# Optimization experiments

Measured on AMD Instinct MI355X. Metric: run time of the kernel, lower is better.

Reference implementation:

```python
import jax, jax.numpy as jnp
import numpy as np

EPS = 1e-5
K = 32  # hardcoded k in SamplingGrouping.forward
S1, S2 = 512, 256  # samples


def conv_bn_relu(x, w, gamma, beta):
    # x: [B, C, L]; w: [O, C] (conv1d kernel_size=1, no bias)
    y = jnp.einsum('bcl,oc->bol', x, w)
    # BatchNorm1d in training mode: stats over (batch, length)
    mean = y.mean(axis=(0, 2), keepdims=True)
    var = y.var(axis=(0, 2), keepdims=True)
    yn = (y - mean) * jax.lax.rsqrt(var + EPS)
    return jax.nn.relu(yn * gamma[None, :, None] + beta[None, :, None])


def fps(coords, s):
    # Farthest point sampling; coords [B, N, 3] -> idx [B, s] (deterministic start at 0)
    B, N, _ = coords.shape
    init_idx = jnp.zeros((B,), jnp.int32)

    def body(carry, _):
        dist, last = carry
        p = jnp.take_along_axis(coords, last[:, None, None], axis=1)  # [B,1,3]
        d = jnp.sum((coords - p) ** 2, axis=-1)                        # [B,N]
        dist = jnp.minimum(dist, d)
        nxt = jnp.argmax(dist, axis=-1).astype(jnp.int32)
        return (dist, nxt), nxt

    (_, _), rest = jax.lax.scan(
        body, (jnp.full((B, N), 1e10, coords.dtype), init_idx), None, length=s - 1)
    return jnp.concatenate([init_idx[None, :], rest], axis=0).T  # [B, s]


def index_points(pts, idx):
    # pts [B,N,D], idx [B,...] int -> [B,...,D]
    return jax.vmap(lambda p, i: p[i])(pts, idx)


def sample_and_knn_group(s, k, coords, features):
    # coords [B,N,3], features [B,N,D] -> new_xyz [B,s,3], agg [B,s,k,2D]
    fps_idx = fps(coords, s)
    new_xyz = index_points(coords, fps_idx)      # [B,s,3]
    new_feat = index_points(features, fps_idx)   # [B,s,D]
    # squared distances [B,s,N]
    d = (jnp.sum(new_xyz ** 2, -1, keepdims=True)
         - 2.0 * jnp.einsum('bsc,bnc->bsn', new_xyz, coords)
         + jnp.sum(coords ** 2, -1)[:, None, :])
    _, knn_idx = jax.lax.top_k(-d, k)            # [B,s,k] nearest neighbours
    grouped = index_points(features, knn_idx)    # [B,s,k,D]
    grouped = grouped - new_feat[:, :, None, :]
    agg = jnp.concatenate(
        [grouped, jnp.broadcast_to(new_feat[:, :, None, :], grouped.shape)], axis=-1)
    return new_xyz, agg


def sg_block(s, coords, feats_bcn, wa, ga, ba, wb, gb, bb):
    # SamplingGrouping.forward
    feats = jnp.transpose(feats_bcn, (0, 2, 1))                 # [B,N,D]
    new_xyz, nf = sample_and_knn_group(s, K, coords, feats)     # [B,s,k,2D]
    b, s_, k, d = nf.shape
    nf = jnp.transpose(nf, (0, 1, 3, 2)).reshape(b * s_, d, k)  # [b*s, d, k]
    nf = conv_bn_relu(nf, wa, ga, ba)
    nf = conv_bn_relu(nf, wb, gb, bb)
    nf = nf.max(axis=2)                                         # adaptive_max_pool1d(.,1)
    nf = jnp.transpose(nf.reshape(b, s_, -1), (0, 2, 1))        # [b, O, s]
    return new_xyz, nf


def setup_inputs() -> dict:
    key = jax.random.key(0)
    ks = jax.random.split(key, 8)
    B, N = 32, 8192
    sc = 0.05
    inp = {
        'x': jax.random.normal(ks[0], (B, 3, N), jnp.float32),
        'w1': jax.random.normal(ks[1], (64, 3), jnp.float32) * sc,
        'g1': jnp.ones((64,), jnp.float32), 'b1': jnp.zeros((64,), jnp.float32),
        'w2': jax.random.normal(ks[2], (64, 64), jnp.float32) * sc,
        'g2': jnp.ones((64,), jnp.float32), 'b2': jnp.zeros((64,), jnp.float32),
        's1wa': jax.random.normal(ks[3], (128, 128), jnp.float32) * sc,
        's1ga': jnp.ones((128,), jnp.float32), 's1ba': jnp.zeros((128,), jnp.float32),
        's1wb': jax.random.normal(ks[4], (128, 128), jnp.float32) * sc,
        's1gb': jnp.ones((128,), jnp.float32), 's1bb': jnp.zeros((128,), jnp.float32),
        's2wa': jax.random.normal(ks[5], (256, 256), jnp.float32) * sc,
        's2ga': jnp.ones((256,), jnp.float32), 's2ba': jnp.zeros((256,), jnp.float32),
        's2wb': jax.random.normal(ks[6], (256, 256), jnp.float32) * sc,
        's2gb': jnp.ones((256,), jnp.float32), 's2bb': jnp.zeros((256,), jnp.float32),
    }
    return inp


def reference(x, w1, g1, b1, w2, g2, b2,
              s1wa, s1ga, s1ba, s1wb, s1gb, s1bb,
              s2wa, s2ga, s2ba, s2wb, s2gb, s2bb):
    xyz = jnp.transpose(x[:, :3, :], (0, 2, 1))  # [B,N,3]
    f = conv_bn_relu(x, w1, g1, b1)
    f = conv_bn_relu(f, w2, g2, b2)              # [B,64,N]
    xyz1, f1 = sg_block(S1, xyz, f, s1wa, s1ga, s1ba, s1wb, s1gb, s1bb)   # [B,128,S1]
    _, f2 = sg_block(S2, xyz1, f1, s2wa, s2ga, s2ba, s2wb, s2gb, s2bb)    # [B,256,S2]
    return f2
```

## Files before the change

### kernel.cpp

```cpp
#include <hip/hip_runtime.h>
#include <hip/hip_bf16.h>

#define NB 32
#define NP 8192

__device__ __forceinline__ float dist3(float ax, float ay, float az,
                                       float bx, float by, float bz) {
#pragma clang fp contract(off)
  float dx = ax - bx, dy = ay - by, dz = az - bz;
  return dx * dx + dy * dy + dz * dz;
}
__device__ __forceinline__ float sumsq3(float x, float y, float z) {
#pragma clang fp contract(off)
  return x * x + y * y + z * z;
}
__device__ __forceinline__ float knndist(float qx, float qy, float qz, float qq,
                                         float cx, float cy, float cz) {
#pragma clang fp contract(off)
  float dot = qx * cx + qy * cy + qz * cz;
  float cc = cx * cx + cy * cy + cz * cz;
  return (qq - 2.0f * dot) + cc;
}

__global__ void k_transpose(const float* __restrict__ w, float* __restrict__ wT,
                            int O, int Dd) {
  int i = blockIdx.x * 256 + threadIdx.x;
  if (i < O * Dd) {
    int o = i / Dd, d = i - o * Dd;
    wT[d * O + o] = w[i];
  }
}

__global__ void k_wdiff(const float* __restrict__ w, float* __restrict__ WdT,
                        int O, int D) {
  int i = blockIdx.x * 256 + threadIdx.x;
  if (i < D * O) {
    int d = i / O, o = i - d * O;
    WdT[i] = w[o * 2 * D + D + d] - w[o * 2 * D + d];
  }
}

__global__ __launch_bounds__(256) void k_s1a(const float* __restrict__ x,
                                             const float* __restrict__ w1,
                                             float* __restrict__ xyz,
                                             float* __restrict__ y1) {
  __shared__ float w1s[192];
  int t = threadIdx.x;
  if (t < 192) w1s[t] = w1[t];
  int gid = blockIdx.x * 256 + t;
  int b = gid >> 13, n = gid & (NP - 1);
  __syncthreads();
  const size_t xb = (size_t)b * 3 * NP;
  float x0 = x[xb + n], x1 = x[xb + NP + n], x2 = x[xb + 2 * NP + n];
  xyz[(size_t)gid * 3 + 0] = x0;
  xyz[(size_t)gid * 3 + 1] = x1;
  xyz[(size_t)gid * 3 + 2] = x2;
  float* yo = y1 + (size_t)gid * 64;
#pragma unroll
  for (int o = 0; o < 64; o += 4) {
    float4 v;
    v.x = x0 * w1s[(o + 0) * 3] + x1 * w1s[(o + 0) * 3 + 1] + x2 * w1s[(o + 0) * 3 + 2];
    v.y = x0 * w1s[(o + 1) * 3] + x1 * w1s[(o + 1) * 3 + 1] + x2 * w1s[(o + 1) * 3 + 2];
    v.z = x0 * w1s[(o + 2) * 3] + x1 * w1s[(o + 2) * 3 + 1] + x2 * w1s[(o + 2) * 3 + 2];
    v.w = x0 * w1s[(o + 3) * 3] + x1 * w1s[(o + 3) * 3 + 1] + x2 * w1s[(o + 3) * 3 + 2];
    *(float4*)&yo[o] = v;
  }
}

__global__ __launch_bounds__(256) void k_colstats(const float* __restrict__ buf,
                                                  size_t ME4, float* __restrict__ part) {
  __shared__ float red[128];
  int t = threadIdx.x;
  if (t < 128) red[t] = 0.f;
  float s[4] = {0.f, 0.f, 0.f, 0.f}, q[4] = {0.f, 0.f, 0.f, 0.f};
  size_t stride = (size_t)gridDim.x * 256;
  size_t i0 = (size_t)blockIdx.x * 256 + t;
  int c0 = (int)((i0 * 4) & 63);
  for (size_t i = i0; i < ME4; i += stride) {
    float4 v = ((const float4*)buf)[i];
    s[0] += v.x; q[0] += v.x * v.x;
    s[1] += v.y; q[1] += v.y * v.y;
    s[2] += v.z; q[2] += v.z * v.z;
    s[3] += v.w; q[3] += v.w * v.w;
  }
  __syncthreads();
#pragma unroll
  for (int j = 0; j < 4; ++j) {
    atomicAdd(&red[c0 + j], s[j]);
    atomicAdd(&red[64 + c0 + j], q[j]);
  }
  __syncthreads();
  if (t < 128) atomicAdd(&part[(size_t)(blockIdx.x & 63) * 128 + t], red[t]);
}

__global__ void k_bnfinal(const float* __restrict__ part, const float* __restrict__ gamma,
                          const float* __restrict__ beta, float invcnt, int C,
                          float* __restrict__ sc) {
  int c = threadIdx.x;
  if (c >= C) return;
  float s = 0.f, q = 0.f;
  for (int p = 0; p < 64; ++p) {
    s += part[(size_t)p * 2 * C + c];
    q += part[(size_t)p * 2 * C + C + c];
  }
  float mean = s * invcnt;
  float var = fmaxf(q * invcnt - mean * mean, 0.f);
  float scale = gamma[c] * rsqrtf(var + 1e-5f);
  sc[c] = scale;
  sc[C + c] = beta[c] - mean * scale;
}

__global__ __launch_bounds__(256) void k_s1c(const float* __restrict__ y1,
                                             const float* __restrict__ w2T,
                                             const float* __restrict__ sc1,
                                             float* __restrict__ y2) {
  __shared__ __align__(16) float f1[64 * 65];
  __shared__ __align__(16) float w2s[64 * 64];
  __shared__ float scs[128];
  int t = threadIdx.x;
  if (t < 128) scs[t] = sc1[t];
  for (int i = t; i < 4096; i += 256) w2s[i] = w2T[i];
  size_t base = (size_t)blockIdx.x * 4096;
  __syncthreads();
  for (int i = t; i < 4096; i += 256) {
    int p = i >> 6, c = i & 63;
    float v = y1[base + i];
    v = fmaxf(0.f, v * scs[c] + scs[64 + c]);
    f1[p * 65 + c] = v;
  }
  __syncthreads();
  int pq = t & 15, oq = t >> 4;
  int p0 = pq * 4, o0 = oq * 4;
  float ac[4][4] = {};
  for (int c = 0; c < 64; ++c) {
    float4 wv = *(const float4*)&w2s[c * 64 + o0];
    float a0 = f1[(p0 + 0) * 65 + c];
    float a1 = f1[(p0 + 1) * 65 + c];
    float a2 = f1[(p0 + 2) * 65 + c];
    float a3 = f1[(p0 + 3) * 65 + c];
    ac[0][0] += a0 * wv.x; ac[0][1] += a0 * wv.y; ac[0][2] += a0 * wv.z; ac[0][3] += a0 * wv.w;
    ac[1][0] += a1 * wv.x; ac[1][1] += a1 * wv.y; ac[1][2] += a1 * wv.z; ac[1][3] += a1 * wv.w;
    ac[2][0] += a2 * wv.x; ac[2][1] += a2 * wv.y; ac[2][2] += a2 * wv.z; ac[2][3] += a2 * wv.w;
    ac[3][0] += a3 * wv.x; ac[3][1] += a3 * wv.y; ac[3][2] += a3 * wv.z; ac[3][3] += a3 * wv.w;
  }
#pragma unroll
  for (int i2 = 0; i2 < 4; ++i2) {
    float4 v = {ac[i2][0], ac[i2][1], ac[i2][2], ac[i2][3]};
    *(float4*)&y2[base + (size_t)(p0 + i2) * 64 + o0] = v;
  }
}

__global__ __launch_bounds__(256) void k_s1e(float* __restrict__ y2,
                                             const float* __restrict__ sc2, size_t ME4) {
  __shared__ float scs[128];
  int t = threadIdx.x;
  if (t < 128) scs[t] = sc2[t];
  __syncthreads();
  size_t stride = (size_t)gridDim.x * 256;
  for (size_t i = (size_t)blockIdx.x * 256 + t; i < ME4; i += stride) {
    float4 v = ((float4*)y2)[i];
    int c0 = (int)((i * 4) & 63);
    v.x = fmaxf(0.f, v.x * scs[c0 + 0] + scs[64 + c0 + 0]);
    v.y = fmaxf(0.f, v.y * scs[c0 + 1] + scs[64 + c0 + 1]);
    v.z = fmaxf(0.f, v.z * scs[c0 + 2] + scs[64 + c0 + 2]);
    v.w = fmaxf(0.f, v.w * scs[c0 + 3] + scs[64 + c0 + 3]);
    ((float4*)y2)[i] = v;
  }
}

template <int N, int S, int PPT>
__global__ __launch_bounds__(N / PPT) void k_fps(const float* __restrict__ xyz,
                                                 int* __restrict__ fidx,
                                                 float* __restrict__ sxyz) {
  constexpr int T = N / PPT;
  constexpr int NW = T / 64;
  __shared__ float cl[N * 3];
  __shared__ float wv[2][NW];
  __shared__ int wi[2][NW];
  const int t = threadIdx.x;
  const int b = blockIdx.x;
  const float* base = xyz + (size_t)b * N * 3;
  for (int i = t; i < 3 * N; i += T) cl[i] = base[i];
  __syncthreads();
  float cx[PPT], cy[PPT], cz[PPT], dist[PPT];
#pragma unroll
  for (int j = 0; j < PPT; ++j) {
    int n = t + j * T;
    cx[j] = cl[n * 3 + 0];
    cy[j] = cl[n * 3 + 1];
    cz[j] = cl[n * 3 + 2];
    dist[j] = 1e10f;
  }
  float px = cl[0], py = cl[1], pz = cl[2];
  if (t == 0) {
    fidx[(size_t)b * S] = 0;
    sxyz[(size_t)b * S * 3 + 0] = px;
    sxyz[(size_t)b * S * 3 + 1] = py;
    sxyz[(size_t)b * S * 3 + 2] = pz;
  }
  int par = 0;
  for (int it = 1; it < S; ++it) {
    float bv = -1.0f;
    int bi = 0x7FFFFFFF;
#pragma unroll
    for (int j = 0; j < PPT; ++j) {
      float d = dist3(cx[j], cy[j], cz[j], px, py, pz);
      float dj = fminf(dist[j], d);
      dist[j] = dj;
      if (dj > bv) { bv = dj; bi = t + j * T; }
    }
#pragma unroll
    for (int off = 32; off > 0; off >>= 1) {
      float ov = __shfl_xor(bv, off);
      int oi = __shfl_xor(bi, off);
      if (ov > bv || (ov == bv && oi < bi)) { bv = ov; bi = oi; }
    }
    if ((t & 63) == 0) { wv[par][t >> 6] = bv; wi[par][t >> 6] = bi; }
    __syncthreads();
    float v = wv[par][0];
    int ii = wi[par][0];
#pragma unroll
    for (int w = 1; w < NW; ++w) {
      float ov = wv[par][w];
      int oi = wi[par][w];
      if (ov > v || (ov == v && oi < ii)) { v = ov; ii = oi; }
    }
    px = cl[ii * 3 + 0]; py = cl[ii * 3 + 1]; pz = cl[ii * 3 + 2];
    if (t == 0) {
      fidx[(size_t)b * S + it] = ii;
      sxyz[((size_t)b * S + it) * 3 + 0] = px;
      sxyz[((size_t)b * S + it) * 3 + 1] = py;
      sxyz[((size_t)b * S + it) * 3 + 2] = pz;
    }
    par ^= 1;
  }
}

template <int NPT>
__global__ __launch_bounds__(256) void k_knn(const float* __restrict__ cxyz,
                                             const float* __restrict__ qxyz, int S,
                                             int* __restrict__ knn) {
  constexpr int N = NPT * 256;
  __shared__ float wv[2][4];
  __shared__ int wi[2][4];
  const int t = threadIdx.x;
  const int bs = blockIdx.x;
  const int b = bs / S;
  float qx = qxyz[(size_t)bs * 3 + 0];
  float qy = qxyz[(size_t)bs * 3 + 1];
  float qz = qxyz[(size_t)bs * 3 + 2];
  float qq = sumsq3(qx, qy, qz);
  const float* cb = cxyz + (size_t)b * N * 3;
  float ds[NPT];
  float lmin = 3.0e38f;
  int li = 0x7FFFFFFF;
#pragma unroll
  for (int j = 0; j < NPT; ++j) {
    int n = t + j * 256;
    float d = knndist(qx, qy, qz, qq, cb[(size_t)n * 3], cb[(size_t)n * 3 + 1],
                      cb[(size_t)n * 3 + 2]);
    ds[j] = d;
    if (d < lmin) { lmin = d; li = n; }
  }
  int par = 0;
  for (int r = 0; r < 32; ++r) {
    float bv = lmin;
    int bi = li;
#pragma unroll
    for (int off = 32; off > 0; off >>= 1) {
      float ov = __shfl_xor(bv, off);
      int oi = __shfl_xor(bi, off);
      if (ov < bv || (ov == bv && oi < bi)) { bv = ov; bi = oi; }
    }
    if ((t & 63) == 0) { wv[par][t >> 6] = bv; wi[par][t >> 6] = bi; }
    __syncthreads();
    float v = wv[par][0];
    int ii = wi[par][0];
#pragma unroll
    for (int w = 1; w < 4; ++w) {
      float ov = wv[par][w];
      int oi = wi[par][w];
      if (ov < v || (ov == v && oi < ii)) { v = ov; ii = oi; }
    }
    if (t == 0) knn[(size_t)bs * 32 + r] = ii;
    if (li == ii) {
#pragma unroll
      for (int j = 0; j < NPT; ++j)
        if (t + j * 256 == ii) ds[j] = 3.0e38f;
      lmin = 3.0e38f;
      li = 0x7FFFFFFF;
#pragma unroll
      for (int j = 0; j < NPT; ++j)
        if (ds[j] < lmin) { lmin = ds[j]; li = t + j * 256; }
    }
    par ^= 1;
  }
}

#define KP 36
__device__ __forceinline__ int swzcol(int d, int k) {
  return (k & 3) | ((((unsigned(k) >> 2) ^ (unsigned(d) >> 2)) & 7) << 2);
}

template <int DR, int O, int NT, int CH>
__device__ __forceinline__ void sg_gemm(const float* __restrict__ X,
                                        const float* __restrict__ WT,
                                        float* __restrict__ wch, int t, int o0, int kq,
                                        float (&ac)[4][4]) {
  for (int dc = 0; dc < DR; dc += CH) {
    __syncthreads();
    for (int i = t; i < CH * O; i += NT) wch[i] = WT[(size_t)dc * O + i];
    __syncthreads();
#pragma unroll 8
    for (int dd = 0; dd < CH; ++dd) {
      int d = dc + dd;
      const float4 wvv = *(const float4*)&wch[dd * O + o0];
      const float4 av = *(const float4*)&X[d * KP + ((kq ^ ((d >> 2) & 7)) << 2)];
      ac[0][0] += wvv.x * av.x; ac[0][1] += wvv.x * av.y; ac[0][2] += wvv.x * av.z; ac[0][3] += wvv.x * av.w;
      ac[1][0] += wvv.y * av.x; ac[1][1] += wvv.y * av.y; ac[1][2] += wvv.y * av.z; ac[1][3] += wvv.y * av.w;
      ac[2][0] += wvv.z * av.x; ac[2][1] += wvv.z * av.y; ac[2][2] += wvv.z * av.z; ac[2][3] += wvv.z * av.w;
      ac[3][0] += wvv.w * av.x; ac[3][1] += wvv.w * av.y; ac[3][2] += wvv.w * av.z; ac[3][3] += wvv.w * av.w;
    }
  }
}

template <int D, int NT>
__device__ __forceinline__ void sg_gatherV(const float* __restrict__ f, int Nf, int b,
                                           const int* __restrict__ nidx,
                                           float* __restrict__ V, int t) {
  constexpr int K = 32, DQ = D / 4;
  const float4* f4 = (const float4*)f;
  for (int idx = t; idx < K * DQ; idx += NT) {
    int k = idx / DQ, dq = idx - k * DQ;
    float4 v = f4[((size_t)b * Nf + nidx[k]) * DQ + dq];
    int d0 = dq * 4;
    V[(d0 + 0) * KP + swzcol(d0 + 0, k)] = v.x;
    V[(d0 + 1) * KP + swzcol(d0 + 1, k)] = v.y;
    V[(d0 + 2) * KP + swzcol(d0 + 2, k)] = v.z;
    V[(d0 + 3) * KP + swzcol(d0 + 3, k)] = v.w;
  }
}

template <int D, int O>
__device__ __forceinline__ void sg_corr(const float* __restrict__ WdT,
                                        const float* __restrict__ fqs, int o0, int kq,
                                        float (&c)[4]) {
  c[0] = c[1] = c[2] = c[3] = 0.f;
  for (int d = kq * (D / 8); d < (kq + 1) * (D / 8); ++d) {
    float qv = fqs[d];
    float4 wd = *(const float4*)&WdT[(size_t)d * O + o0];
    c[0] += wd.x * qv; c[1] += wd.y * qv; c[2] += wd.z * qv; c[3] += wd.w * qv;
  }
#pragma unroll
  for (int m = 1; m < 8; m <<= 1) {
    c[0] += __shfl_xor(c[0], m);
    c[1] += __shfl_xor(c[1], m);
    c[2] += __shfl_xor(c[2], m);
    c[3] += __shfl_xor(c[3], m);
  }
}

template <int D, int NT>
__global__ __launch_bounds__(NT) void k_sgA(const float* __restrict__ f, int Nf, int S,
                                            const int* __restrict__ fpsidx,
                                            const int* __restrict__ knn,
                                            const float* __restrict__ waT,
                                            const float* __restrict__ WdT,
                                            float* __restrict__ statsOut) {
  constexpr int D2 = 2 * D, O = D2, K = 32, CH = 16, DQ = D / 4;
  __shared__ __align__(16) float V[D * KP];
  __shared__ __align__(16) float wch[CH * O];
  __shared__ __align__(16) float fqs[D];
  __shared__ int nidx[K];
  __shared__ float red[2 * O];
  const int t = threadIdx.x;
  const int bs = blockIdx.x;
  const int b = bs / S;
  const int qi = fpsidx[bs];
  if (t < K) nidx[t] = knn[(size_t)bs * K + t];
  const float4* f4 = (const float4*)f;
  for (int i = t; i < DQ; i += NT)
    ((float4*)fqs)[i] = f4[((size_t)b * Nf + qi) * DQ + i];
  __syncthreads();
  sg_gatherV<D, NT>(f, Nf, b, nidx, V, t);
  const int oq = t >> 3, kq = t & 7;
  const int o0 = oq * 4;
  float c[4];
  sg_corr<D, O>(WdT, fqs, o0, kq, c);
  float acc[4][4];
#pragma unroll
  for (int i2 = 0; i2 < 4; ++i2)
#pragma unroll
    for (int j = 0; j < 4; ++j) acc[i2][j] = c[i2];
  sg_gemm<D, O, NT, CH>(V, waT, wch, t, o0, kq, acc);
#pragma unroll
  for (int i2 = 0; i2 < 4; ++i2) {
    float sv = acc[i2][0] + acc[i2][1] + acc[i2][2] + acc[i2][3];
    float sq = acc[i2][0] * acc[i2][0] + acc[i2][1] * acc[i2][1] +
               acc[i2][2] * acc[i2][2] + acc[i2][3] * acc[i2][3];
#pragma unroll
    for (int m = 1; m < 8; m <<= 1) {
      sv += __shfl_xor(sv, m);
      sq += __shfl_xor(sq, m);
    }
    if (kq == 0) {
      red[o0 + i2] = sv;
      red[O + o0 + i2] = sq;
    }
  }
  __syncthreads();
  float* slot = statsOut + (size_t)(bs & 63) * (2 * O);
  for (int i = t; i < 2 * O; i += NT) atomicAdd(&slot[i], red[i]);
}

template <int D, int NT>
__global__ __launch_bounds__(NT) void k_sgAB(const float* __restrict__ f, int Nf, int S,
                                             const int* __restrict__ fpsidx,
                                             const int* __restrict__ knn,
                                             const float* __restrict__ waT,
                                             const float* __restrict__ WdT,
                                             const float* __restrict__ wbT,
                                             const float* __restrict__ bnA,
                                             float* __restrict__ statsOut,
                                             float* __restrict__ mm) {
  constexpr int D2 = 2 * D, O = D2, K = 32, CH = 16, DQ = D / 4;
  __shared__ __align__(16) float V[D * KP];
  __shared__ __align__(16) float zb[O * KP];
  __shared__ __align__(16) float wch[CH * O];
  __shared__ __align__(16) float fqs[D];
  __shared__ int nidx[K];
  __shared__ float red[2 * O];
  __shared__ float scb[2 * O];
  const int t = threadIdx.x;
  const int bs = blockIdx.x;
  const int b = bs / S;
  const int qi = fpsidx[bs];
  if (t < K) nidx[t] = knn[(size_t)bs * K + t];
  const float4* f4 = (const float4*)f;
  for (int i = t; i < DQ; i += NT)
    ((float4*)fqs)[i] = f4[((size_t)b * Nf + qi) * DQ + i];
  for (int i = t; i < 2 * O; i += NT) scb[i] = bnA[i];
  __syncthreads();
  sg_gatherV<D, NT>(f, Nf, b, nidx, V, t);
  const int oq = t >> 3, kq = t & 7;
  const int o0 = oq * 4;
  float c[4];
  sg_corr<D, O>(WdT, fqs, o0, kq, c);
  float acc[4][4];
#pragma unroll
  for (int i2 = 0; i2 < 4; ++i2)
#pragma unroll
    for (int j = 0; j < 4; ++j) acc[i2][j] = c[i2];
  sg_gemm<D, O, NT, CH>(V, waT, wch, t, o0, kq, acc);
#pragma unroll
  for (int i2 = 0; i2 < 4; ++i2) {
    float sA = scb[o0 + i2], tA = scb[O + o0 + i2];
    float4 z;
    z.x = fmaxf(0.f, acc[i2][0] * sA + tA);
    z.y = fmaxf(0.f, acc[i2][1] * sA + tA);
    z.z = fmaxf(0.f, acc[i2][2] * sA + tA);
    z.w = fmaxf(0.f, acc[i2][3] * sA + tA);
    *(float4*)&zb[(o0 + i2) * KP + ((kq ^ (oq & 7)) << 2)] = z;
  }
  float ac2[4][4];
#pragma unroll
  for (int i2 = 0; i2 < 4; ++i2)
#pragma unroll
    for (int j = 0; j < 4; ++j) ac2[i2][j] = 0.f;
  sg_gemm<O, O, NT, CH>(zb, wbT, wch, t, o0, kq, ac2);
  float* mrow = mm + (size_t)bs * 2 * O;
#pragma unroll
  for (int i2 = 0; i2 < 4; ++i2) {
    float sv = ac2[i2][0] + ac2[i2][1] + ac2[i2][2] + ac2[i2][3];
    float sq = ac2[i2][0] * ac2[i2][0] + ac2[i2][1] * ac2[i2][1] +
               ac2[i2][2] * ac2[i2][2] + ac2[i2][3] * ac2[i2][3];
    float mx = fmaxf(fmaxf(ac2[i2][0], ac2[i2][1]), fmaxf(ac2[i2][2], ac2[i2][3]));
    float mn = fminf(fminf(ac2[i2][0], ac2[i2][1]), fminf(ac2[i2][2], ac2[i2][3]));
#pragma unroll
    for (int m = 1; m < 8; m <<= 1) {
      sv += __shfl_xor(sv, m);
      sq += __shfl_xor(sq, m);
      mx = fmaxf(mx, __shfl_xor(mx, m));
      mn = fminf(mn, __shfl_xor(mn, m));
    }
    if (kq == 0) {
      red[o0 + i2] = sv;
      red[O + o0 + i2] = sq;
      mrow[o0 + i2] = mx;
      mrow[O + o0 + i2] = mn;
    }
  }
  __syncthreads();
  float* slot = statsOut + (size_t)(bs & 63) * (2 * O);
  for (int i = t; i < 2 * O; i += NT) atomicAdd(&slot[i], red[i]);
}

template <int O>
__global__ __launch_bounds__(256) void k_fin(const float* __restrict__ mm,
                                             const float* __restrict__ bnB, int S,
                                             float* __restrict__ out, int finalOut) {
  int idx = blockIdx.x * 256 + threadIdx.x;
  int o, bs;
  if (finalOut) {
    int s = idx % S;
    int bo = idx / S;
    o = bo % O;
    int b = bo / O;
    bs = b * S + s;
  } else {
    o = idx % O;
    bs = idx / O;
  }
  float sB = bnB[o], tB = bnB[O + o];
  const float* r = mm + (size_t)bs * 2 * O;
  float ext = (sB >= 0.f) ? r[o] : r[O + o];
  out[idx] = fmaxf(0.f, sB * ext + tB);
}

extern "C" void kernel_launch(void* const* d_in, const int* in_sizes, int n_in,
                              void* d_out, int out_size, void* d_ws, size_t ws_size,
                              hipStream_t stream) {
  (void)in_sizes; (void)n_in; (void)out_size; (void)ws_size;
  const float* x    = (const float*)d_in[0];
  const float* w1   = (const float*)d_in[1];
  const float* g1   = (const float*)d_in[2];
  const float* b1   = (const float*)d_in[3];
  const float* w2   = (const float*)d_in[4];
  const float* g2   = (const float*)d_in[5];
  const float* b2   = (const float*)d_in[6];
  const float* s1wa = (const float*)d_in[7];
  const float* s1ga = (const float*)d_in[8];
  const float* s1ba = (const float*)d_in[9];
  const float* s1wb = (const float*)d_in[10];
  const float* s1gb = (const float*)d_in[11];
  const float* s1bb = (const float*)d_in[12];
  const float* s2wa = (const float*)d_in[13];
  const float* s2ga = (const float*)d_in[14];
  const float* s2ba = (const float*)d_in[15];
  const float* s2wb = (const float*)d_in[16];
  const float* s2gb = (const float*)d_in[17];
  const float* s2bb = (const float*)d_in[18];
  float* out = (float*)d_out;

  char* wsp = (char*)d_ws;
  size_t off = 0;
  auto alloc = [&](size_t floats) {
    void* p = wsp + off;
    off += ((floats * 4 + 255) & ~(size_t)255);
    return p;
  };
  float* xyz  = (float*)alloc(786432);
  float* y1   = (float*)alloc(16777216);
  float* y2f  = y1;
  float* f1f  = (float*)alloc(2097152);
  float* xyz1 = (float*)alloc(49152);
  float* xyz2 = (float*)alloc(24576);
  int* fi1    = (int*)alloc(16384);
  int* fi2    = (int*)alloc(8192);
  int* kn1    = (int*)alloc(524288);
  int* kn2    = (int*)alloc(262144);
  float* w2T  = (float*)alloc(4096);
  float* waT1 = (float*)alloc(16384);
  float* wbT1 = (float*)alloc(16384);
  float* waT2 = (float*)alloc(65536);
  float* wbT2 = (float*)alloc(65536);
  float* WdT1 = (float*)alloc(8192);
  float* WdT2 = (float*)alloc(32768);
  float* stats = (float*)alloc(116480);
  float* part_s1 = stats;
  float* part_s2 = stats + 8192;
  float* partA1  = stats + 16384;
  float* partB1  = stats + 32768;
  float* partA2  = stats + 49152;
  float* partB2  = stats + 81920;
  float* sc1  = stats + 114688;
  float* sc2  = sc1 + 128;
  float* bnA1 = sc2 + 128;
  float* bnB1 = bnA1 + 256;
  float* bnA2 = bnB1 + 256;
  float* bnB2 = bnA2 + 512;
  float* mm = (float*)alloc(4194304);

  hipMemsetAsync(stats, 0, (size_t)114688 * 4, stream);

  k_transpose<<<(64 * 64 + 255) / 256, 256, 0, stream>>>(w2, w2T, 64, 64);
  k_transpose<<<(128 * 128 + 255) / 256, 256, 0, stream>>>(s1wa, waT1, 128, 128);
  k_transpose<<<(128 * 128 + 255) / 256, 256, 0, stream>>>(s1wb, wbT1, 128, 128);
  k_transpose<<<(256 * 256 + 255) / 256, 256, 0, stream>>>(s2wa, waT2, 256, 256);
  k_transpose<<<(256 * 256 + 255) / 256, 256, 0, stream>>>(s2wb, wbT2, 256, 256);
  k_wdiff<<<(64 * 128 + 255) / 256, 256, 0, stream>>>(s1wa, WdT1, 128, 64);
  k_wdiff<<<(128 * 256 + 255) / 256, 256, 0, stream>>>(s2wa, WdT2, 256, 128);

  const size_t MN = (size_t)NB * NP;
  k_s1a<<<(int)(MN / 256), 256, 0, stream>>>(x, w1, xyz, y1);
  k_colstats<<<1024, 256, 0, stream>>>(y1, MN * 16, part_s1);
  k_bnfinal<<<1, 64, 0, stream>>>(part_s1, g1, b1, 1.f / (float)MN, 64, sc1);
  k_s1c<<<(int)(MN / 64), 256, 0, stream>>>(y1, w2T, sc1, y2f);
  k_colstats<<<1024, 256, 0, stream>>>(y2f, MN * 16, part_s2);
  k_bnfinal<<<1, 64, 0, stream>>>(part_s2, g2, b2, 1.f / (float)MN, 64, sc2);
  k_s1e<<<2048, 256, 0, stream>>>(y2f, sc2, MN * 16);

  k_fps<NP, 512, 16><<<NB, 512, 0, stream>>>(xyz, fi1, xyz1);
  k_knn<32><<<NB * 512, 256, 0, stream>>>(xyz, xyz1, 512, kn1);

  const float icA1 = 1.f / (32.f * 512.f * 32.f);
  const float icA2 = 1.f / (32.f * 256.f * 32.f);

  k_sgA<64, 256><<<NB * 512, 256, 0, stream>>>(y2f, NP, 512, fi1, kn1, waT1, WdT1, partA1);
  k_bnfinal<<<1, 128, 0, stream>>>(partA1, s1ga, s1ba, icA1, 128, bnA1);
  k_sgAB<64, 256><<<NB * 512, 256, 0, stream>>>(y2f, NP, 512, fi1, kn1, waT1, WdT1,
                                                wbT1, bnA1, partB1, mm);
  k_bnfinal<<<1, 128, 0, stream>>>(partB1, s1gb, s1bb, icA1, 128, bnB1);
  k_fin<128><<<8192, 256, 0, stream>>>(mm, bnB1, 512, f1f, 0);

  k_fps<512, 256, 1><<<NB, 512, 0, stream>>>(xyz1, fi2, xyz2);
  k_knn<2><<<NB * 256, 256, 0, stream>>>(xyz1, xyz2, 256, kn2);

  k_sgA<128, 512><<<NB * 256, 512, 0, stream>>>(f1f, 512, 256, fi2, kn2, waT2, WdT2, partA2);
  k_bnfinal<<<1, 256, 0, stream>>>(partA2, s2ga, s2ba, icA2, 256, bnA2);
  k_sgAB<128, 512><<<NB * 256, 512, 0, stream>>>(f1f, 512, 256, fi2, kn2, waT2, WdT2,
                                                 wbT2, bnA2, partB2, mm);
  k_bnfinal<<<1, 256, 0, stream>>>(partB2, s2gb, s2bb, icA2, 256, bnB2);
  k_fin<256><<<8192, 256, 0, stream>>>(mm, bnB2, 256, out, 1);
}
```

Baseline: 4.345 ms.

## Add single-wave FPS, retune FPS blocks, widen stat slots, share LDS in sgAB

```diff
diff --git a/kernel.cpp b/kernel.cpp
--- a/kernel.cpp
+++ b/kernel.cpp
@@ -94,12 +94,12 @@
 }
 
 __global__ void k_bnfinal(const float* __restrict__ part, const float* __restrict__ gamma,
-                          const float* __restrict__ beta, float invcnt, int C,
+                          const float* __restrict__ beta, float invcnt, int C, int P,
                           float* __restrict__ sc) {
   int c = threadIdx.x;
   if (c >= C) return;
   float s = 0.f, q = 0.f;
-  for (int p = 0; p < 64; ++p) {
+  for (int p = 0; p < P; ++p) {
     s += part[(size_t)p * 2 * C + c];
     q += part[(size_t)p * 2 * C + C + c];
   }
@@ -233,6 +233,58 @@
       sxyz[((size_t)b * S + it) * 3 + 2] = pz;
     }
     par ^= 1;
+  }
+}
+
+template <int N, int S, int PPT>
+__global__ __launch_bounds__(64) void k_fpsw(const float* __restrict__ xyz,
+                                             int* __restrict__ fidx,
+                                             float* __restrict__ sxyz) {
+  __shared__ float cl[N * 3];
+  const int t = threadIdx.x;
+  const int b = blockIdx.x;
+  const float* base = xyz + (size_t)b * N * 3;
+  for (int i = t; i < 3 * N; i += 64) cl[i] = base[i];
+  __syncthreads();
+  float cx[PPT], cy[PPT], cz[PPT], dist[PPT];
+#pragma unroll
+  for (int j = 0; j < PPT; ++j) {
+    int n = t + j * 64;
+    cx[j] = cl[n * 3 + 0];
+    cy[j] = cl[n * 3 + 1];
+    cz[j] = cl[n * 3 + 2];
+    dist[j] = 1e10f;
+  }
+  float px = cl[0], py = cl[1], pz = cl[2];
+  if (t == 0) {
+    fidx[(size_t)b * S] = 0;
+    sxyz[(size_t)b * S * 3 + 0] = px;
+    sxyz[(size_t)b * S * 3 + 1] = py;
+    sxyz[(size_t)b * S * 3 + 2] = pz;
+  }
+  for (int it = 1; it < S; ++it) {
+    float bv = -1.0f;
+    int bi = 0x7FFFFFFF;
+#pragma unroll
+    for (int j = 0; j < PPT; ++j) {
+      float d = dist3(cx[j], cy[j], cz[j], px, py, pz);
+      float dj = fminf(dist[j], d);
+      dist[j] = dj;
+      if (dj > bv) { bv = dj; bi = t + j * 64; }
+    }
+#pragma unroll
+    for (int off = 32; off > 0; off >>= 1) {
+      float ov = __shfl_xor(bv, off);
+      int oi = __shfl_xor(bi, off);
+      if (ov > bv || (ov == bv && oi < bi)) { bv = ov; bi = oi; }
+    }
+    px = cl[bi * 3 + 0]; py = cl[bi * 3 + 1]; pz = cl[bi * 3 + 2];
+    if (t == 0) {
+      fidx[(size_t)b * S + it] = bi;
+      sxyz[((size_t)b * S + it) * 3 + 0] = px;
+      sxyz[((size_t)b * S + it) * 3 + 1] = py;
+      sxyz[((size_t)b * S + it) * 3 + 2] = pz;
+    }
   }
 }
 
@@ -409,7 +461,7 @@
     }
   }
   __syncthreads();
-  float* slot = statsOut + (size_t)(bs & 63) * (2 * O);
+  float* slot = statsOut + (size_t)(bs & 255) * (2 * O);
   for (int i = t; i < 2 * O; i += NT) atomicAdd(&slot[i], red[i]);
 }
 
@@ -423,9 +475,8 @@
                                              const float* __restrict__ bnA,
                                              float* __restrict__ statsOut,
                                              float* __restrict__ mm) {
-  constexpr int D2 = 2 * D, O = D2, K = 32, CH = 16, DQ = D / 4;
-  __shared__ __align__(16) float V[D * KP];
-  __shared__ __align__(16) float zb[O * KP];
+  constexpr int D2 = 2 * D, O = D2, K = 32, CH = 32, DQ = D / 4;
+  __shared__ __align__(16) float VZ[O * KP];
   __shared__ __align__(16) float wch[CH * O];
   __shared__ __align__(16) float fqs[D];
   __shared__ int nidx[K];
@@ -441,7 +492,7 @@
     ((float4*)fqs)[i] = f4[((size_t)b * Nf + qi) * DQ + i];
   for (int i = t; i < 2 * O; i += NT) scb[i] = bnA[i];
   __syncthreads();
-  sg_gatherV<D, NT>(f, Nf, b, nidx, V, t);
+  sg_gatherV<D, NT>(f, Nf, b, nidx, VZ, t);
   const int oq = t >> 3, kq = t & 7;
   const int o0 = oq * 4;
   float c[4];
@@ -451,7 +502,8 @@
   for (int i2 = 0; i2 < 4; ++i2)
 #pragma unroll
     for (int j = 0; j < 4; ++j) acc[i2][j] = c[i2];
-  sg_gemm<D, O, NT, CH>(V, waT, wch, t, o0, kq, acc);
+  sg_gemm<D, O, NT, CH>(VZ, waT, wch, t, o0, kq, acc);
+  __syncthreads();
 #pragma unroll
   for (int i2 = 0; i2 < 4; ++i2) {
     float sA = scb[o0 + i2], tA = scb[O + o0 + i2];
@@ -460,14 +512,14 @@
     z.y = fmaxf(0.f, acc[i2][1] * sA + tA);
     z.z = fmaxf(0.f, acc[i2][2] * sA + tA);
     z.w = fmaxf(0.f, acc[i2][3] * sA + tA);
-    *(float4*)&zb[(o0 + i2) * KP + ((kq ^ (oq & 7)) << 2)] = z;
+    *(float4*)&VZ[(o0 + i2) * KP + ((kq ^ (oq & 7)) << 2)] = z;
   }
   float ac2[4][4];
 #pragma unroll
   for (int i2 = 0; i2 < 4; ++i2)
 #pragma unroll
     for (int j = 0; j < 4; ++j) ac2[i2][j] = 0.f;
-  sg_gemm<O, O, NT, CH>(zb, wbT, wch, t, o0, kq, ac2);
+  sg_gemm<O, O, NT, CH>(VZ, wbT, wch, t, o0, kq, ac2);
   float* mrow = mm + (size_t)bs * 2 * O;
 #pragma unroll
   for (int i2 = 0; i2 < 4; ++i2) {
@@ -491,7 +543,7 @@
     }
   }
   __syncthreads();
-  float* slot = statsOut + (size_t)(bs & 63) * (2 * O);
+  float* slot = statsOut + (size_t)(bs & 255) * (2 * O);
   for (int i = t; i < 2 * O; i += NT) atomicAdd(&slot[i], red[i]);
 }
 
@@ -566,14 +618,14 @@
   float* wbT2 = (float*)alloc(65536);
   float* WdT1 = (float*)alloc(8192);
   float* WdT2 = (float*)alloc(32768);
-  float* stats = (float*)alloc(116480);
+  float* stats = (float*)alloc(411392);
   float* part_s1 = stats;
   float* part_s2 = stats + 8192;
   float* partA1  = stats + 16384;
-  float* partB1  = stats + 32768;
-  float* partA2  = stats + 49152;
-  float* partB2  = stats + 81920;
-  float* sc1  = stats + 114688;
+  float* partB1  = stats + 81920;
+  float* partA2  = stats + 147456;
+  float* partB2  = stats + 278528;
+  float* sc1  = stats + 409600;
   float* sc2  = sc1 + 128;
   float* bnA1 = sc2 + 128;
   float* bnB1 = bnA1 + 256;
@@ -581,7 +633,7 @@
   float* bnB2 = bnA2 + 512;
   float* mm = (float*)alloc(4194304);
 
-  hipMemsetAsync(stats, 0, (size_t)114688 * 4, stream);
+  hipMemsetAsync(stats, 0, (size_t)409600 * 4, stream);
 
   k_transpose<<<(64 * 64 + 255) / 256, 256, 0, stream>>>(w2, w2T, 64, 64);
   k_transpose<<<(128 * 128 + 255) / 256, 256, 0, stream>>>(s1wa, waT1, 128, 128);
@@ -594,32 +646,32 @@
   const size_t MN = (size_t)NB * NP;
   k_s1a<<<(int)(MN / 256), 256, 0, stream>>>(x, w1, xyz, y1);
   k_colstats<<<1024, 256, 0, stream>>>(y1, MN * 16, part_s1);
-  k_bnfinal<<<1, 64, 0, stream>>>(part_s1, g1, b1, 1.f / (float)MN, 64, sc1);
+  k_bnfinal<<<1, 64, 0, stream>>>(part_s1, g1, b1, 1.f / (float)MN, 64, 64, sc1);
   k_s1c<<<(int)(MN / 64), 256, 0, stream>>>(y1, w2T, sc1, y2f);
   k_colstats<<<1024, 256, 0, stream>>>(y2f, MN * 16, part_s2);
-  k_bnfinal<<<1, 64, 0, stream>>>(part_s2, g2, b2, 1.f / (float)MN, 64, sc2);
+  k_bnfinal<<<1, 64, 0, stream>>>(part_s2, g2, b2, 1.f / (float)MN, 64, 64, sc2);
   k_s1e<<<2048, 256, 0, stream>>>(y2f, sc2, MN * 16);
 
-  k_fps<NP, 512, 16><<<NB, 512, 0, stream>>>(xyz, fi1, xyz1);
+  k_fps<NP, 512, 32><<<NB, 256, 0, stream>>>(xyz, fi1, xyz1);
   k_knn<32><<<NB * 512, 256, 0, stream>>>(xyz, xyz1, 512, kn1);
 
   const float icA1 = 1.f / (32.f * 512.f * 32.f);
   const float icA2 = 1.f / (32.f * 256.f * 32.f);
 
   k_sgA<64, 256><<<NB * 512, 256, 0, stream>>>(y2f, NP, 512, fi1, kn1, waT1, WdT1, partA1);
-  k_bnfinal<<<1, 128, 0, stream>>>(partA1, s1ga, s1ba, icA1, 128, bnA1);
+  k_bnfinal<<<1, 128, 0, stream>>>(partA1, s1ga, s1ba, icA1, 128, 256, bnA1);
   k_sgAB<64, 256><<<NB * 512, 256, 0, stream>>>(y2f, NP, 512, fi1, kn1, waT1, WdT1,
                                                 wbT1, bnA1, partB1, mm);
-  k_bnfinal<<<1, 128, 0, stream>>>(partB1, s1gb, s1bb, icA1, 128, bnB1);
+  k_bnfinal<<<1, 128, 0, stream>>>(partB1, s1gb, s1bb, icA1, 128, 256, bnB1);
   k_fin<128><<<8192, 256, 0, stream>>>(mm, bnB1, 512, f1f, 0);
 
-  k_fps<512, 256, 1><<<NB, 512, 0, stream>>>(xyz1, fi2, xyz2);
+  k_fpsw<512, 256, 8><<<NB, 64, 0, stream>>>(xyz1, fi2, xyz2);
   k_knn<2><<<NB * 256, 256, 0, stream>>>(xyz1, xyz2, 256, kn2);
 
   k_sgA<128, 512><<<NB * 256, 512, 0, stream>>>(f1f, 512, 256, fi2, kn2, waT2, WdT2, partA2);
-  k_bnfinal<<<1, 256, 0, stream>>>(partA2, s2ga, s2ba, icA2, 256, bnA2);
+  k_bnfinal<<<1, 256, 0, stream>>>(partA2, s2ga, s2ba, icA2, 256, 256, bnA2);
   k_sgAB<128, 512><<<NB * 256, 512, 0, stream>>>(f1f, 512, 256, fi2, kn2, waT2, WdT2,
                                                  wbT2, bnA2, partB2, mm);
-  k_bnfinal<<<1, 256, 0, stream>>>(partB2, s2gb, s2bb, icA2, 256, bnB2);
+  k_bnfinal<<<1, 256, 0, stream>>>(partB2, s2gb, s2bb, icA2, 256, 256, bnB2);
   k_fin<256><<<8192, 256, 0, stream>>>(mm, bnB2, 256, out, 1);
 }
```

Measured after the change: 4.253 ms. 1.02x faster.
